# Optimization experiments

Measured on AMD Instinct MI355X. Metric: run time of the kernel, lower is better.

The kernel has to match this reference:

```python
import jax, jax.numpy as jnp
import numpy as np

NUM_CLASSES = 21
RADIUS = 3          # rmi_radius
POOL = 3            # rmi_pool_size == rmi_pool_stride
PAD = POOL // 2
HALF_D = RADIUS * RADIUS
CLIP_MIN = 1e-6
POS_ALPHA = 5e-4
LAMBDA = 0.5        # loss_weight_lambda, lambda_way=1


def setup_inputs() -> dict:
    key = jax.random.key(0)
    k1, k2 = jax.random.split(key)
    logits_4D = jax.random.normal(k1, (4, NUM_CLASSES, 512, 512), dtype=jnp.float32)
    labels_4D = jax.random.randint(k2, (4, 512, 512), 0, NUM_CLASSES)
    return {"logits_4D": logits_4D, "labels_4D": labels_4D}


def _max_pool(x):
    # F.max_pool2d(kernel=3, stride=3, padding=1); pad value -inf matches torch
    return jax.lax.reduce_window(
        x, -jnp.inf, jax.lax.max,
        window_dimensions=(1, 1, POOL, POOL),
        window_strides=(1, 1, POOL, POOL),
        padding=((0, 0), (0, 0), (PAD, PAD), (PAD, PAD)))


def _map_get_pairs(la, pr, radius):
    # stack radius*radius shifted crops -> [N, C, half_d, new_h, new_w]
    h, w = la.shape[2], la.shape[3]
    nh, nw = h - (radius - 1), w - (radius - 1)
    la_s = jnp.stack([la[:, :, y:y + nh, x:x + nw]
                      for y in range(radius) for x in range(radius)], axis=2)
    pr_s = jnp.stack([pr[:, :, y:y + nh, x:x + nw]
                      for y in range(radius) for x in range(radius)], axis=2)
    return la_s, pr_s


def _log_det_by_cholesky(m):
    chol = jnp.linalg.cholesky(m)
    return 2.0 * jnp.sum(jnp.log(jnp.diagonal(chol, axis1=-2, axis2=-1)), axis=-1)


def _rmi_lower_bound(labels_4D, probs_4D):
    la = _max_pool(labels_4D)
    pr = _max_pool(probs_4D)
    n, c = la.shape[0], la.shape[1]
    la_v, pr_v = _map_get_pairs(la, pr, RADIUS)
    la_v = jax.lax.stop_gradient(la_v.reshape(n, c, HALF_D, -1))   # [N,C,9,M]
    pr_v = pr_v.reshape(n, c, HALF_D, -1)
    eye = jnp.eye(HALF_D, dtype=pr_v.dtype)
    la_v = la_v - la_v.mean(axis=3, keepdims=True)
    pr_v = pr_v - pr_v.mean(axis=3, keepdims=True)
    la_cov = jnp.einsum('ncdm,ncem->ncde', la_v, la_v)             # [N,C,9,9]
    pr_cov = jnp.einsum('ncdm,ncem->ncde', pr_v, pr_v)
    pr_cov_inv = jnp.linalg.inv(pr_cov + eye * POS_ALPHA)
    la_pr_cov = jnp.einsum('ncdm,ncem->ncde', la_v, pr_v)
    appro_var = la_cov - la_pr_cov @ pr_cov_inv @ jnp.swapaxes(la_pr_cov, -2, -1)
    rmi_now = 0.5 * _log_det_by_cholesky(appro_var + eye * POS_ALPHA)  # [N,C]
    rmi_per_class = rmi_now.reshape(-1, NUM_CLASSES).mean(axis=0) / HALF_D
    return jnp.sum(rmi_per_class)


def reference(logits_4D, labels_4D):
    mask = labels_4D < NUM_CLASSES                         # [N,H,W] bool
    maskf = mask.astype(jnp.float32)
    onehot = jax.nn.one_hot(labels_4D * mask, NUM_CLASSES, dtype=jnp.float32)
    onehot = onehot * maskf[..., None]                     # [N,H,W,C]
    logits_flat = jnp.transpose(logits_4D, (0, 2, 3, 1)).reshape(-1, NUM_CLASSES)
    onehot_flat = onehot.reshape(-1, NUM_CLASSES)
    mflat = maskf.reshape(-1, 1)
    # stable BCE-with-logits, weight=mask, reduction='sum'
    bce = (jnp.maximum(logits_flat, 0) - logits_flat * onehot_flat
           + jnp.log1p(jnp.exp(-jnp.abs(logits_flat))))
    valid_pixels = jnp.sum(maskf)
    bce_loss = jnp.sum(bce * mflat) / (valid_pixels + 1.0)
    probs_4D = jax.nn.sigmoid(logits_4D) * maskf[:, None] + CLIP_MIN
    labels_nchw = jnp.transpose(onehot, (0, 3, 1, 2))      # [N,C,H,W]
    rmi_loss = _rmi_lower_bound(labels_nchw, probs_4D)
    return LAMBDA * bce_loss + (1.0 - LAMBDA) * rmi_loss
```

## Files before the change

### kernel.cpp

```cpp
#include <hip/hip_runtime.h>

#define NCLS   21
#define HI     512
#define WI     512
#define PH     171
#define PLANE  (PH*PH)
#define NH     169
#define MPTS   (NH*NH)
#define NBATCH 4
#define NC     (NBATCH*NCLS)
#define ALPHA  5e-4f
#define SPLIT  8

#define OFF_BCE    0
#define OFF_VALID  512
#define OFF_MEANS  1024
#define OFF_COV    7104
#define ZERO_BYTES (OFF_COV + NC*171*4)
#define OFF_LA8    65536
#define OFF_PR     (65536 + ((NC*PLANE + 255)/256)*256)

#define IDX(i,j) ((i)*((i)+1)/2 + (j))
#define KU(d,e)  (9*(d) - ((d)*((d)-1))/2 + ((e)-(d)))

__device__ __forceinline__ float wave_red(float v) {
#pragma unroll
    for (int off = 32; off; off >>= 1) v += __shfl_down(v, off, 64);
    return v;
}

__global__ __launch_bounds__(256) void pool_bce_kernel(
    const float* __restrict__ logits, const int* __restrict__ labels,
    unsigned char* __restrict__ la_pool, float* __restrict__ pr_pool,
    float* __restrict__ meansums, double* __restrict__ bce_part,
    double* __restrict__ valid_part)
{
    const int c = blockIdx.y, n = blockIdx.z;
    const int pos = blockIdx.x * 256 + threadIdx.x;
    const int plane = n * NCLS + c;

    float bce_acc = 0.f, cnt = 0.f;
    float sl[9], sp[9];
#pragma unroll
    for (int d = 0; d < 9; ++d) { sl[d] = 0.f; sp[d] = 0.f; }

    if (pos < PLANE) {
        const int oh = pos / PH, ow = pos - oh * PH;
        const float* lg = logits + (size_t)plane * (HI * WI);
        const int*   lb = labels + (size_t)n * (HI * WI);
        float mx_la = -1.f, mx_pr = -1.f;
        const int r0 = 3 * oh - 1, c0 = 3 * ow - 1;
#pragma unroll
        for (int dy = 0; dy < 3; ++dy) {
            const int r = r0 + dy;
            if (r < 0 || r >= HI) continue;
#pragma unroll
            for (int dx = 0; dx < 3; ++dx) {
                const int cc = c0 + dx;
                if (cc < 0 || cc >= WI) continue;
                const float x  = lg[r * WI + cc];
                const int  lab = lb[r * WI + cc];
                const bool m   = (lab < NCLS);
                const float o  = (m && lab == c) ? 1.f : 0.f;
                const float t  = expf(-fabsf(x));
                const float sig = (x >= 0.f) ? 1.f / (1.f + t) : t / (1.f + t);
                const float prob = (m ? sig : 0.f) + 1e-6f;
                if (m) bce_acc += fmaxf(x, 0.f) - x * o + log1pf(t);
                if (m && c == 0) cnt += 1.f;
                mx_la = fmaxf(mx_la, o);
                mx_pr = fmaxf(mx_pr, prob);
            }
        }
        la_pool[(size_t)plane * PLANE + pos] = (unsigned char)mx_la;
        pr_pool[(size_t)plane * PLANE + pos] = mx_pr;
#pragma unroll
        for (int y = 0; y < 3; ++y)
#pragma unroll
            for (int x = 0; x < 3; ++x) {
                const int d = y * 3 + x;
                if (oh >= y && oh <= y + NH - 1 && ow >= x && ow <= x + NH - 1) {
                    sl[d] += mx_la; sp[d] += mx_pr;
                }
            }
    }

    __shared__ float red[4][20];
    const int lane = threadIdx.x & 63, wid = threadIdx.x >> 6;
    float vals[20];
#pragma unroll
    for (int d = 0; d < 9; ++d) { vals[d] = sl[d]; vals[9 + d] = sp[d]; }
    vals[18] = bce_acc; vals[19] = cnt;
#pragma unroll
    for (int q = 0; q < 20; ++q) {
        const float v = wave_red(vals[q]);
        if (lane == 0) red[wid][q] = v;
    }
    __syncthreads();
    if (threadIdx.x < 20) {
        const float v = red[0][threadIdx.x] + red[1][threadIdx.x]
                      + red[2][threadIdx.x] + red[3][threadIdx.x];
        if (threadIdx.x < 18) {
            atomicAdd(meansums + plane * 18 + threadIdx.x, v);
        } else if (threadIdx.x == 18) {
            const int bid = (blockIdx.z * gridDim.y + blockIdx.y) * gridDim.x + blockIdx.x;
            atomicAdd(bce_part + (bid & 63), (double)v);
        } else if (blockIdx.y == 0) {
            const int bid = blockIdx.z * gridDim.x + blockIdx.x;
            atomicAdd(valid_part + (bid & 63), (double)v);
        }
    }
}

__global__ __launch_bounds__(256, 1) void cov_kernel(
    const unsigned char* __restrict__ la_pool, const float* __restrict__ pr_pool,
    const float* __restrict__ meansums, float* __restrict__ covbuf)
{
    const int nc = blockIdx.x / SPLIT, s = blockIdx.x % SPLIT;
    const unsigned char* la = la_pool + (size_t)nc * PLANE;
    const float*         pr = pr_pool + (size_t)nc * PLANE;

    float ml[9], mp[9];
    const float invM = 1.f / (float)MPTS;
#pragma unroll
    for (int d = 0; d < 9; ++d) {
        ml[d] = meansums[nc * 18 + d]     * invM;
        mp[d] = meansums[nc * 18 + 9 + d] * invM;
    }

    float ll[45], pp[45], lp[81];
#pragma unroll
    for (int k = 0; k < 45; ++k) { ll[k] = 0.f; pp[k] = 0.f; }
#pragma unroll
    for (int k = 0; k < 81; ++k) lp[k] = 0.f;

    for (int m = s * 256 + threadIdx.x; m < MPTS; m += 256 * SPLIT) {
        const int i = m / NH, j = m - i * NH;
        const int base = i * PH + j;
        float lv[9], pv[9];
#pragma unroll
        for (int y = 0; y < 3; ++y)
#pragma unroll
            for (int x = 0; x < 3; ++x) {
                const int d = y * 3 + x;
                lv[d] = (float)la[base + y * PH + x] - ml[d];
                pv[d] = pr[base + y * PH + x] - mp[d];
            }
        int k = 0;
#pragma unroll
        for (int d = 0; d < 9; ++d)
#pragma unroll
            for (int e = d; e < 9; ++e) { ll[k] += lv[d] * lv[e]; pp[k] += pv[d] * pv[e]; ++k; }
#pragma unroll
        for (int d = 0; d < 9; ++d)
#pragma unroll
            for (int e = 0; e < 9; ++e) lp[d * 9 + e] += lv[d] * pv[e];
    }

    __shared__ float red[4][171];
    const int lane = threadIdx.x & 63, wid = threadIdx.x >> 6;
#pragma unroll
    for (int q = 0; q < 45; ++q) { const float v = wave_red(ll[q]); if (!lane) red[wid][q] = v; }
#pragma unroll
    for (int q = 0; q < 45; ++q) { const float v = wave_red(pp[q]); if (!lane) red[wid][45 + q] = v; }
#pragma unroll
    for (int q = 0; q < 81; ++q) { const float v = wave_red(lp[q]); if (!lane) red[wid][90 + q] = v; }
    __syncthreads();
    if (threadIdx.x < 171) {
        const float v = red[0][threadIdx.x] + red[1][threadIdx.x]
                      + red[2][threadIdx.x] + red[3][threadIdx.x];
        atomicAdd(covbuf + nc * 171 + threadIdx.x, v);
    }
}

__global__ __launch_bounds__(128, 1) void final_kernel(
    const float* __restrict__ covbuf, const double* __restrict__ bce_part,
    const double* __restrict__ valid_part, float* __restrict__ out)
{
    const int t = threadIdx.x;
    float rmi = 0.f;
    if (t < NC) {
        const float* cb = covbuf + t * 171;

        float L[45], dinv[9];
#pragma unroll
        for (int k = 0; k < 9; ++k) {
            float s = cb[45 + KU(k, k)] + ALPHA;
#pragma unroll
            for (int p = 0; p < k; ++p) s -= L[IDX(k, p)] * L[IDX(k, p)];
            const float dk = sqrtf(s);
            L[IDX(k, k)] = dk;
            dinv[k] = 1.f / dk;
#pragma unroll
            for (int i = k + 1; i < 9; ++i) {
                float t2 = cb[45 + KU(k, i)];
#pragma unroll
                for (int p = 0; p < k; ++p) t2 -= L[IDX(i, p)] * L[IDX(k, p)];
                L[IDX(i, k)] = t2 * dinv[k];
            }
        }

        float Yv[81];
#pragma unroll
        for (int i = 0; i < 9; ++i)
#pragma unroll
            for (int j = 0; j < 9; ++j) Yv[i * 9 + j] = cb[90 + j * 9 + i];
#pragma unroll
        for (int i = 0; i < 9; ++i)
#pragma unroll
            for (int j = 0; j < 9; ++j) {
                float t2 = Yv[i * 9 + j];
#pragma unroll
                for (int p = 0; p < i; ++p) t2 -= L[IDX(i, p)] * Yv[p * 9 + j];
                Yv[i * 9 + j] = t2 * dinv[i];
            }

        float V[45];
#pragma unroll
        for (int d = 0; d < 9; ++d)
#pragma unroll
            for (int e = d; e < 9; ++e) {
                float s = cb[KU(d, e)];
#pragma unroll
                for (int i = 0; i < 9; ++i) s -= Yv[i * 9 + d] * Yv[i * 9 + e];
                V[KU(d, e)] = s;
            }
        float M2[45];
        float rmi_acc = 0.f;
#pragma unroll
        for (int k = 0; k < 9; ++k) {
            float s = V[KU(k, k)] + ALPHA;
#pragma unroll
            for (int p = 0; p < k; ++p) s -= M2[IDX(k, p)] * M2[IDX(k, p)];
            const float dk = sqrtf(s);
            M2[IDX(k, k)] = dk;
            rmi_acc += logf(dk);
            const float di = 1.f / dk;
#pragma unroll
            for (int i = k + 1; i < 9; ++i) {
                float t2 = V[KU(k, i)];
#pragma unroll
                for (int p = 0; p < k; ++p) t2 -= M2[IDX(i, p)] * M2[IDX(k, p)];
                M2[IDX(i, k)] = t2 * di;
            }
        }
        rmi = rmi_acc;
    }

    __shared__ float red[128];
    red[t] = rmi;
    __syncthreads();
#pragma unroll
    for (int off = 64; off >= 1; off >>= 1) {
        if (t < off) red[t] += red[t + off];
        __syncthreads();
    }
    if (t == 0) {
        double b = 0.0, v = 0.0;
        for (int k = 0; k < 64; ++k) { b += bce_part[k]; v += valid_part[k]; }
        const float bce_loss = (float)(b / (v + 1.0));
        const float rmi_loss = red[0] / (float)(NBATCH * 9);
        out[0] = 0.5f * bce_loss + 0.5f * rmi_loss;
    }
}

extern "C" void kernel_launch(void* const* d_in, const int* in_sizes, int n_in,
                              void* d_out, int out_size, void* d_ws, size_t ws_size,
                              hipStream_t stream)
{
    const float* logits = (const float*)d_in[0];
    const int*   labels = (const int*)d_in[1];
    char* ws = (char*)d_ws;

    double*        bce_part   = (double*)(ws + OFF_BCE);
    double*        valid_part = (double*)(ws + OFF_VALID);
    float*         meansums   = (float*)(ws + OFF_MEANS);
    float*         covbuf     = (float*)(ws + OFF_COV);
    unsigned char* la_pool    = (unsigned char*)(ws + OFF_LA8);
    float*         pr_pool    = (float*)(ws + OFF_PR);

    hipMemsetAsync(ws, 0, ZERO_BYTES, stream);

    dim3 g1((PLANE + 255) / 256, NCLS, NBATCH);
    pool_bce_kernel<<<g1, 256, 0, stream>>>(logits, labels, la_pool, pr_pool,
                                            meansums, bce_part, valid_part);
    cov_kernel<<<NC * SPLIT, 256, 0, stream>>>(la_pool, pr_pool, meansums, covbuf);
    final_kernel<<<1, 128, 0, stream>>>(covbuf, bce_part, valid_part, (float*)d_out);
}
```

Baseline: 295.6 us.

## Split covariance work across waves to cut registers; use fast exp/log/rcp

The covariance kernel now assigns each of the four waves a different block of the 171 covariance terms (la-la, pr-pr, and two halves of la-pr). Each thread then keeps only 45 accumulators instead of 171, and launch bounds allow four blocks per CU to raise occupancy. The cost is redundant loads, since each wave re-reads the la/pr windows, and per-wave atomics replace the shared-memory reduction. The pooling kernel uses __expf, rcp and __logf intrinsics and drops the upper-edge bounds checks, which never trigger because 3*170+1 < 512. The fast math slightly reduces accuracy.

```diff
diff --git a/kernel.cpp b/kernel.cpp
--- a/kernel.cpp
+++ b/kernel.cpp
@@ -53,22 +53,24 @@
 #pragma unroll
         for (int dy = 0; dy < 3; ++dy) {
             const int r = r0 + dy;
-            if (r < 0 || r >= HI) continue;
+            if (r < 0) continue;
 #pragma unroll
             for (int dx = 0; dx < 3; ++dx) {
                 const int cc = c0 + dx;
-                if (cc < 0 || cc >= WI) continue;
-                const float x  = lg[r * WI + cc];
-                const int  lab = lb[r * WI + cc];
-                const bool m   = (lab < NCLS);
-                const float o  = (m && lab == c) ? 1.f : 0.f;
-                const float t  = expf(-fabsf(x));
-                const float sig = (x >= 0.f) ? 1.f / (1.f + t) : t / (1.f + t);
-                const float prob = (m ? sig : 0.f) + 1e-6f;
-                if (m) bce_acc += fmaxf(x, 0.f) - x * o + log1pf(t);
+                if (cc < 0) continue;
+                const float x   = lg[r * WI + cc];
+                const int  lab  = lb[r * WI + cc];
+                const bool m    = (lab < NCLS);
+                const float o   = (m && lab == c) ? 1.f : 0.f;
+                const float t   = __expf(-fabsf(x));
+                const float u   = 1.f + t;
+                const float rc  = __builtin_amdgcn_rcpf(u);
+                const float lgu = __logf(u);
+                const float sig = (x >= 0.f) ? rc : t * rc;
+                if (m) bce_acc += fmaxf(x, 0.f) - x * o + lgu;
                 if (m && c == 0) cnt += 1.f;
                 mx_la = fmaxf(mx_la, o);
-                mx_pr = fmaxf(mx_pr, prob);
+                mx_pr = fmaxf(mx_pr, (m ? sig : 0.f) + 1e-6f);
             }
         }
         la_pool[(size_t)plane * PLANE + pos] = (unsigned char)mx_la;
@@ -111,11 +113,12 @@
     }
 }
 
-__global__ __launch_bounds__(256, 1) void cov_kernel(
+__global__ __launch_bounds__(256, 4) void cov_kernel(
     const unsigned char* __restrict__ la_pool, const float* __restrict__ pr_pool,
     const float* __restrict__ meansums, float* __restrict__ covbuf)
 {
     const int nc = blockIdx.x / SPLIT, s = blockIdx.x % SPLIT;
+    const int lane = threadIdx.x & 63, wid = threadIdx.x >> 6;
     const unsigned char* la = la_pool + (size_t)nc * PLANE;
     const float*         pr = pr_pool + (size_t)nc * PLANE;
 
@@ -127,48 +130,75 @@
         mp[d] = meansums[nc * 18 + 9 + d] * invM;
     }
 
-    float ll[45], pp[45], lp[81];
-#pragma unroll
-    for (int k = 0; k < 45; ++k) { ll[k] = 0.f; pp[k] = 0.f; }
-#pragma unroll
-    for (int k = 0; k < 81; ++k) lp[k] = 0.f;
-
-    for (int m = s * 256 + threadIdx.x; m < MPTS; m += 256 * SPLIT) {
-        const int i = m / NH, j = m - i * NH;
-        const int base = i * PH + j;
-        float lv[9], pv[9];
-#pragma unroll
-        for (int y = 0; y < 3; ++y)
-#pragma unroll
-            for (int x = 0; x < 3; ++x) {
-                const int d = y * 3 + x;
-                lv[d] = (float)la[base + y * PH + x] - ml[d];
-                pv[d] = pr[base + y * PH + x] - mp[d];
-            }
-        int k = 0;
-#pragma unroll
-        for (int d = 0; d < 9; ++d)
-#pragma unroll
-            for (int e = d; e < 9; ++e) { ll[k] += lv[d] * lv[e]; pp[k] += pv[d] * pv[e]; ++k; }
-#pragma unroll
-        for (int d = 0; d < 9; ++d)
-#pragma unroll
-            for (int e = 0; e < 9; ++e) lp[d * 9 + e] += lv[d] * pv[e];
-    }
-
-    __shared__ float red[4][171];
-    const int lane = threadIdx.x & 63, wid = threadIdx.x >> 6;
-#pragma unroll
-    for (int q = 0; q < 45; ++q) { const float v = wave_red(ll[q]); if (!lane) red[wid][q] = v; }
-#pragma unroll
-    for (int q = 0; q < 45; ++q) { const float v = wave_red(pp[q]); if (!lane) red[wid][45 + q] = v; }
-#pragma unroll
-    for (int q = 0; q < 81; ++q) { const float v = wave_red(lp[q]); if (!lane) red[wid][90 + q] = v; }
-    __syncthreads();
-    if (threadIdx.x < 171) {
-        const float v = red[0][threadIdx.x] + red[1][threadIdx.x]
-                      + red[2][threadIdx.x] + red[3][threadIdx.x];
-        atomicAdd(covbuf + nc * 171 + threadIdx.x, v);
+    float acc[45];
+#pragma unroll
+    for (int k = 0; k < 45; ++k) acc[k] = 0.f;
+
+    for (int m = s * 64 + lane; m < MPTS; m += 64 * SPLIT) {
+        const int i = m / NH;
+        const int base = m + 2 * i;
+        if (wid == 0) {
+            float lv[9];
+#pragma unroll
+            for (int y = 0; y < 3; ++y)
+#pragma unroll
+                for (int x = 0; x < 3; ++x)
+                    lv[y * 3 + x] = (float)la[base + y * PH + x] - ml[y * 3 + x];
+            int k = 0;
+#pragma unroll
+            for (int d = 0; d < 9; ++d)
+#pragma unroll
+                for (int e = d; e < 9; ++e) { acc[k++] += lv[d] * lv[e]; }
+        } else if (wid == 1) {
+            float pv[9];
+#pragma unroll
+            for (int y = 0; y < 3; ++y)
+#pragma unroll
+                for (int x = 0; x < 3; ++x)
+                    pv[y * 3 + x] = pr[base + y * PH + x] - mp[y * 3 + x];
+            int k = 0;
+#pragma unroll
+            for (int d = 0; d < 9; ++d)
+#pragma unroll
+                for (int e = d; e < 9; ++e) { acc[k++] += pv[d] * pv[e]; }
+        } else if (wid == 2) {
+            float lv[4], pv[9];
+#pragma unroll
+            for (int d = 0; d < 4; ++d)
+                lv[d] = (float)la[base + (d / 3) * PH + (d % 3)] - ml[d];
+#pragma unroll
+            for (int y = 0; y < 3; ++y)
+#pragma unroll
+                for (int x = 0; x < 3; ++x)
+                    pv[y * 3 + x] = pr[base + y * PH + x] - mp[y * 3 + x];
+#pragma unroll
+            for (int d = 0; d < 4; ++d)
+#pragma unroll
+                for (int e = 0; e < 9; ++e) acc[d * 9 + e] += lv[d] * pv[e];
+        } else {
+            float lv[5], pv[9];
+#pragma unroll
+            for (int d = 4; d < 9; ++d)
+                lv[d - 4] = (float)la[base + (d / 3) * PH + (d % 3)] - ml[d];
+#pragma unroll
+            for (int y = 0; y < 3; ++y)
+#pragma unroll
+                for (int x = 0; x < 3; ++x)
+                    pv[y * 3 + x] = pr[base + y * PH + x] - mp[y * 3 + x];
+#pragma unroll
+            for (int d = 0; d < 5; ++d)
+#pragma unroll
+                for (int e = 0; e < 9; ++e) acc[d * 9 + e] += lv[d] * pv[e];
+        }
+    }
+
+    const int nacc = (wid == 2) ? 36 : 45;
+    const int obase = (wid == 0) ? 0 : (wid == 1) ? 45 : (wid == 2) ? 90 : 126;
+#pragma unroll
+    for (int k = 0; k < 45; ++k) {
+        if (k >= nacc) break;
+        const float v = wave_red(acc[k]);
+        if (lane == 0) atomicAdd(covbuf + nc * 171 + obase + k, v);
     }
 }
 
```

New measurement: 440.3 us. 1.49x slower.
